# Kernel optimization log

Hardware: AMD Instinct MI355X
Metric: run time of the kernel (lower is better)

The kernel has to match this reference:

```python
import math
import jax, jax.numpy as jnp
import numpy as np

B, S, D = 2, 2048, 4096
H = 32
HD = D // H  # 128
CLIP_QKV = 8.0
ALIBI_BIAS_MAX = 8
LN_EPS = 1e-5


def _get_alibi_slopes(total_num_heads: int, alibi_bias_max: int) -> np.ndarray:
    next_pow2 = 2 ** math.ceil(math.log2(total_num_heads))
    m = np.arange(1, next_pow2 + 1, dtype=np.float32) * (alibi_bias_max / next_pow2)
    slopes = 1.0 / np.power(2.0, m)
    if next_pow2 != total_num_heads:
        slopes = np.concatenate([slopes[1::2], slopes[::2]])[:total_num_heads]
    return slopes


ALIBI_SLOPES = jnp.asarray(_get_alibi_slopes(H, ALIBI_BIAS_MAX))  # [H]


def _layernorm(x, w, b):
    mu = jnp.mean(x, axis=-1, keepdims=True)
    var = jnp.mean(jnp.square(x - mu), axis=-1, keepdims=True)
    return (x - mu) * jax.lax.rsqrt(var + LN_EPS) * w + b


def setup_inputs() -> dict:
    key = jax.random.key(0)
    ks = jax.random.split(key, 3)
    scale_in = 1.0 / math.sqrt(D)
    return {
        "hidden_states": jax.random.normal(ks[0], (B, S, D), jnp.float32),
        "Wqkv": jax.random.normal(ks[1], (D, 3 * D), jnp.float32) * scale_in,
        "Wout": jax.random.normal(ks[2], (D, D), jnp.float32) * scale_in,
        "q_ln_w": jnp.ones((D,), jnp.float32),
        "q_ln_b": jnp.zeros((D,), jnp.float32),
        "k_ln_w": jnp.ones((D,), jnp.float32),
        "k_ln_b": jnp.zeros((D,), jnp.float32),
    }


def reference(hidden_states, Wqkv, Wout, q_ln_w, q_ln_b, k_ln_w, k_ln_b):
    # QKV projection + clamp
    qkv = jnp.clip(hidden_states @ Wqkv, -CLIP_QKV, CLIP_QKV)  # [B,S,3D]
    q, k, v = jnp.split(qkv, [D, 2 * D], axis=-1)
    # QK LayerNorm over full d_model (as in MPT qk_ln)
    q = _layernorm(q, q_ln_w, q_ln_b)
    k = _layernorm(k, k_ln_w, k_ln_b)
    # split heads
    q = q.reshape(B, S, H, HD)
    k = k.reshape(B, S, H, HD)
    v = v.reshape(B, S, H, HD)
    scale = HD ** (-0.5)
    scores = jnp.einsum("bqhd,bkhd->bhqk", q, k) * scale  # [B,H,S,S]
    # ALiBi bias: -slope * (i - j), causal mask j <= i
    pos = jnp.arange(S)
    dist = pos[:, None] - pos[None, :]  # [S,S], i - j
    bias = -ALIBI_SLOPES[:, None, None] * dist.astype(jnp.float32)  # [H,S,S]
    causal = dist >= 0
    scores = jnp.where(causal[None, None], scores + bias[None], -jnp.inf)
    attn = jax.nn.softmax(scores, axis=-1)
    out = jnp.einsum("bhqk,bkhd->bqhd", attn, v).reshape(B, S, D)
    return out @ Wout
```

## Files before the change

### kernel.cpp

```cpp
#include <hip/hip_runtime.h>
#include <hip/hip_bf16.h>
#include <stdint.h>

#define BB 2
#define SS 2048
#define DD 4096
#define HH 32
#define HDD 128

typedef unsigned short u16;
typedef unsigned int u32;

constexpr float CLIPV  = 8.0f;
constexpr float LN_EPS_ = 1e-5f;
constexpr float SCALE_ = 0.08838834764831845f;
constexpr float LOG2E_ = 1.4426950408889634f;

using f32x4 = __attribute__((ext_vector_type(4))) float;
using s16x8 = __attribute__((ext_vector_type(8))) short;

__device__ inline u16 f2bf(float f) {
  union { float f; u32 u; } v; v.f = f;
  u32 r = (v.u + 0x7FFFu + ((v.u >> 16) & 1u)) >> 16;
  return (u16)r;
}
__device__ inline float bf2f(u16 u) {
  union { u32 u; float f; } v; v.u = ((u32)u) << 16;
  return v.f;
}

typedef __attribute__((address_space(1))) void gvoid;
typedef __attribute__((address_space(3))) void lvoid;
__device__ inline void gload_lds16(const void* g, void* l) {
  __builtin_amdgcn_global_load_lds((gvoid*)g, (lvoid*)l, 16, 0, 0);
}

__device__ inline f32x4 mfma16(s16x8 a, s16x8 b, f32x4 c) {
  return __builtin_amdgcn_mfma_f32_16x16x32_bf16(a, b, c, 0, 0, 0);
}

__global__ void k_cvt_bf16(const float* __restrict__ in, u16* __restrict__ out, int nvec) {
  int i = blockIdx.x * 256 + threadIdx.x;
  if (i >= nvec) return;
  float4 a = ((const float4*)in)[i * 2];
  float4 b = ((const float4*)in)[i * 2 + 1];
  u16 tmp[8];
  tmp[0] = f2bf(a.x); tmp[1] = f2bf(a.y); tmp[2] = f2bf(a.z); tmp[3] = f2bf(a.w);
  tmp[4] = f2bf(b.x); tmp[5] = f2bf(b.y); tmp[6] = f2bf(b.z); tmp[7] = f2bf(b.w);
  ((uint4*)out)[i] = *(const uint4*)tmp;
}

__global__ void k_transpose_cvt(const float* __restrict__ src, u16* __restrict__ dst, int R, int C) {
  __shared__ float tile[32][33];
  int c0 = blockIdx.x * 32, r0 = blockIdx.y * 32;
  int tx = threadIdx.x & 31, ty = threadIdx.x >> 5;
  #pragma unroll
  for (int i = 0; i < 32; i += 8)
    tile[ty + i][tx] = src[(size_t)(r0 + ty + i) * C + (c0 + tx)];
  __syncthreads();
  #pragma unroll
  for (int i = 0; i < 32; i += 8)
    dst[(size_t)(c0 + ty + i) * R + (r0 + tx)] = f2bf(tile[tx][ty + i]);
}

__device__ __forceinline__ void stage_half(u16* ldsHalf, const u16* g, int K, int tid) {
  #pragma unroll
  for (int it = 0; it < 2; ++it) {
    int p = (it << 9) + tid;
    int row = p >> 3;
    int slotk = (p & 7) ^ (row & 7);
    gload_lds16(g + (size_t)row * K + (slotk << 3), ldsHalf + ((size_t)p << 3));
  }
}

#define MFMA_QUAD(MB, JB)                                                     \
  _Pragma("unroll")                                                           \
  for (int i_ = 0; i_ < 4; ++i_) {                                            \
    _Pragma("unroll")                                                         \
    for (int jj_ = 0; jj_ < 2; ++jj_) {                                       \
      acc[(MB) + i_][(JB) + jj_] =                                            \
          mfma16(aF[i_][0], bF[(JB) + jj_][0], acc[(MB) + i_][(JB) + jj_]);   \
      acc[(MB) + i_][(JB) + jj_] =                                            \
          mfma16(aF[i_][1], bF[(JB) + jj_][1], acc[(MB) + i_][(JB) + jj_]);   \
    }                                                                         \
  }

template <int EPI>
__launch_bounds__(512)
__global__ void k_gemm256(const u16* __restrict__ A, const u16* __restrict__ Bt,
                          void* __restrict__ Cout, int M, int N, int K, int nBY) {
  __shared__ u16 sA[32768];
  __shared__ u16 sB[32768];
  const int tid = threadIdx.x;
  const int lane = tid & 63, w = tid >> 6;
  const int wm = w >> 2, wn = w & 3;
  const int lg = lane >> 4, lc = lane & 15;

  const int nwg = gridDim.x;
  const int cpx = nwg >> 3;
  const int id2 = (blockIdx.x & 7) * cpx + (blockIdx.x >> 3);
  const int bx = id2 / nBY, by = id2 % nBY;
  const int m0 = by * 256, n0 = bx * 256;

  const int NT = K >> 6;
  const u16* gA = A  + (size_t)m0 * K;
  const u16* gB = Bt + (size_t)n0 * K;

  const int xt0 = ((lg) ^ (lc & 7)) * 8;
  const int xt1 = xt0 ^ 32;
  const int rowoff = lc * 64;

  f32x4 acc[8][4];
  #pragma unroll
  for (int i = 0; i < 8; ++i)
    #pragma unroll
    for (int j = 0; j < 4; ++j) acc[i][j] = (f32x4){0.f, 0.f, 0.f, 0.f};

  stage_half(sA,        gA,                    K, tid);
  stage_half(sA + 8192, gA + (size_t)128 * K,  K, tid);
  stage_half(sB,        gB,                    K, tid);
  stage_half(sB + 8192, gB + (size_t)128 * K,  K, tid);
  if (NT > 1) {
    stage_half(sB + 16384,        gB + 64,                   K, tid);
    stage_half(sB + 16384 + 8192, gB + (size_t)128 * K + 64, K, tid);
    stage_half(sA + 16384,        gA + 64,                   K, tid);
    asm volatile("s_waitcnt vmcnt(6)" ::: "memory");
  } else {
    asm volatile("s_waitcnt vmcnt(0)" ::: "memory");
  }
  __builtin_amdgcn_s_barrier();

  for (int t = 0; t < NT; ++t) {
    const int d = t & 1;
    u16* aB = sA + d * 16384 + wm * 8192;
    u16* bB = sB + d * 16384 + (wn >> 1) * 8192 + (wn & 1) * 4096;

    s16x8 aF[4][2], bF[4][2];

    #pragma unroll
    for (int j = 0; j < 2; ++j) {
      bF[j][0] = *(const s16x8*)(bB + j * 1024 + rowoff + xt0);
      bF[j][1] = *(const s16x8*)(bB + j * 1024 + rowoff + xt1);
    }
    #pragma unroll
    for (int i = 0; i < 4; ++i) {
      aF[i][0] = *(const s16x8*)(aB + i * 1024 + rowoff + xt0);
      aF[i][1] = *(const s16x8*)(aB + i * 1024 + rowoff + xt1);
    }
    if (t + 1 < NT)
      stage_half(sA + (d ^ 1) * 16384 + 8192,
                 gA + (size_t)128 * K + (size_t)(t + 1) * 64, K, tid);
    __builtin_amdgcn_s_barrier();
    asm volatile("s_waitcnt lgkmcnt(0)" ::: "memory");
    __builtin_amdgcn_s_setprio(1);
    MFMA_QUAD(0, 0)
    __builtin_amdgcn_s_setprio(0);
    __builtin_amdgcn_s_barrier();

    #pragma unroll
    for (int j = 2; j < 4; ++j) {
      bF[j][0] = *(const s16x8*)(bB + j * 1024 + rowoff + xt0);
      bF[j][1] = *(const s16x8*)(bB + j * 1024 + rowoff + xt1);
    }
    __builtin_amdgcn_s_barrier();
    asm volatile("s_waitcnt lgkmcnt(0)" ::: "memory");
    __builtin_amdgcn_s_setprio(1);
    MFMA_QUAD(0, 2)
    __builtin_amdgcn_s_setprio(0);
    __builtin_amdgcn_s_barrier();

    #pragma unroll
    for (int i = 0; i < 4; ++i) {
      aF[i][0] = *(const s16x8*)(aB + 4096 + i * 1024 + rowoff + xt0);
      aF[i][1] = *(const s16x8*)(aB + 4096 + i * 1024 + rowoff + xt1);
    }
    if (t + 2 < NT) {
      stage_half(sB + d * 16384,        gB + (size_t)(t + 2) * 64,                   K, tid);
      stage_half(sB + d * 16384 + 8192, gB + (size_t)128 * K + (size_t)(t + 2) * 64, K, tid);
    }
    __builtin_amdgcn_s_barrier();
    asm volatile("s_waitcnt lgkmcnt(0)" ::: "memory");
    __builtin_amdgcn_s_setprio(1);
    MFMA_QUAD(4, 0)
    __builtin_amdgcn_s_setprio(0);
    __builtin_amdgcn_s_barrier();

    if (t + 2 < NT)
      stage_half(sA + d * 16384, gA + (size_t)(t + 2) * 64, K, tid);
    __builtin_amdgcn_s_barrier();
    asm volatile("s_waitcnt lgkmcnt(0)" ::: "memory");
    __builtin_amdgcn_s_setprio(1);
    MFMA_QUAD(4, 2)
    __builtin_amdgcn_s_setprio(0);
    if (t + 2 < NT) asm volatile("s_waitcnt vmcnt(6)" ::: "memory");
    else            asm volatile("s_waitcnt vmcnt(0)" ::: "memory");
    __builtin_amdgcn_s_barrier();
  }

  #pragma unroll
  for (int i = 0; i < 8; ++i)
    #pragma unroll
    for (int j = 0; j < 4; ++j)
      #pragma unroll
      for (int r = 0; r < 4; ++r) {
        int m = m0 + wm * 128 + i * 16 + lg * 4 + r;
        int n = n0 + wn * 64 + j * 16 + lc;
        float v = acc[i][j][r];
        if (EPI == 0) {
          v = fminf(fmaxf(v, -CLIPV), CLIPV);
          ((u16*)Cout)[(size_t)m * N + n] = f2bf(v);
        } else {
          ((float*)Cout)[(size_t)m * N + n] = v;
        }
      }
}

__device__ inline void unpack8(uint4 u, float* f) {
  const u16* p = (const u16*)&u;
  #pragma unroll
  for (int j = 0; j < 8; ++j) f[j] = bf2f(p[j]);
}

__global__ void k_ln_reorder(const u16* __restrict__ qkv,
                             const float* __restrict__ qw, const float* __restrict__ qb,
                             const float* __restrict__ kw, const float* __restrict__ kb,
                             u16* __restrict__ Qo, u16* __restrict__ Ko) {
  const int row = blockIdx.x;
  const int b = row >> 11, s = row & 2047;
  const int t = threadIdx.x;
  const int lane = t & 63, w = t >> 6;
  const uint4* base = (const uint4*)(qkv + (size_t)row * (3 * DD));

  __shared__ float redsum[8], redss[8];

  uint4 q4[2], k4[2];
  q4[0] = base[t];        q4[1] = base[256 + t];
  k4[0] = base[512 + t];  k4[1] = base[768 + t];

  float qx[16], kx[16];
  unpack8(q4[0], qx); unpack8(q4[1], qx + 8);
  unpack8(k4[0], kx); unpack8(k4[1], kx + 8);

  float qs = 0.f, qss = 0.f, ks = 0.f, kss = 0.f;
  #pragma unroll
  for (int i = 0; i < 16; ++i) {
    qs += qx[i]; qss += qx[i] * qx[i];
    ks += kx[i]; kss += kx[i] * kx[i];
  }
  #pragma unroll
  for (int off = 1; off < 64; off <<= 1) {
    qs  += __shfl_xor(qs, off);  qss += __shfl_xor(qss, off);
    ks  += __shfl_xor(ks, off);  kss += __shfl_xor(kss, off);
  }
  if (lane == 0) { redsum[w] = qs; redss[w] = qss; redsum[4 + w] = ks; redss[4 + w] = kss; }
  __syncthreads();
  float qsum = redsum[0] + redsum[1] + redsum[2] + redsum[3];
  float qs2  = redss[0]  + redss[1]  + redss[2]  + redss[3];
  float ksum = redsum[4] + redsum[5] + redsum[6] + redsum[7];
  float ks2  = redss[4]  + redss[5]  + redss[6]  + redss[7];
  const float inv = 1.0f / (float)DD;
  float qmu = qsum * inv, qvar = qs2 * inv - qmu * qmu;
  float kmu = ksum * inv, kvar = ks2 * inv - kmu * kmu;
  float qrs = rsqrtf(qvar + LN_EPS_);
  float krs = rsqrtf(kvar + LN_EPS_);

  #pragma unroll
  for (int ch = 0; ch < 2; ++ch) {
    int c0 = ch * 2048 + t * 8;
    int hh = c0 >> 7, hd0 = c0 & 127;
    size_t idx = (((size_t)b * HH + hh) * SS + s) * HDD + hd0;
    {
      float4 w0 = *(const float4*)(qw + c0), w1 = *(const float4*)(qw + c0 + 4);
      float4 b0 = *(const float4*)(qb + c0), b1 = *(const float4*)(qb + c0 + 4);
      float wa[8] = {w0.x, w0.y, w0.z, w0.w, w1.x, w1.y, w1.z, w1.w};
      float ba[8] = {b0.x, b0.y, b0.z, b0.w, b1.x, b1.y, b1.z, b1.w};
      u16 tmp[8];
      #pragma unroll
      for (int j = 0; j < 8; ++j)
        tmp[j] = f2bf((qx[ch * 8 + j] - qmu) * qrs * wa[j] + ba[j]);
      *(uint4*)(Qo + idx) = *(const uint4*)tmp;
    }
    {
      float4 w0 = *(const float4*)(kw + c0), w1 = *(const float4*)(kw + c0 + 4);
      float4 b0 = *(const float4*)(kb + c0), b1 = *(const float4*)(kb + c0 + 4);
      float wa[8] = {w0.x, w0.y, w0.z, w0.w, w1.x, w1.y, w1.z, w1.w};
      float ba[8] = {b0.x, b0.y, b0.z, b0.w, b1.x, b1.y, b1.z, b1.w};
      u16 tmp[8];
      #pragma unroll
      for (int j = 0; j < 8; ++j)
        tmp[j] = f2bf((kx[ch * 8 + j] - kmu) * krs * wa[j] + ba[j]);
      *(uint4*)(Ko + idx) = *(const uint4*)tmp;
    }
  }
}

__global__ void k_transpose_v(const u16* __restrict__ qkv, u16* __restrict__ Vt) {
  __shared__ u16 ls[64 * 65];
  const int s0 = blockIdx.x * 64;
  const int hd0 = blockIdx.y * 64;
  const int bh = blockIdx.z;
  const int b = bh >> 5, h = bh & 31;
  const int t = threadIdx.x;
  const u16* src = qkv + (size_t)(b * SS + s0) * (3 * DD) + 2 * DD + h * HDD + hd0;
  #pragma unroll
  for (int it = 0; it < 4; ++it) {
    int idx = it * 256 + t;
    int sr = idx >> 4, hc = idx & 15;
    uint2 v = *(const uint2*)(src + (size_t)sr * (3 * DD) + hc * 4);
    const u16* pv = (const u16*)&v;
    #pragma unroll
    for (int j = 0; j < 4; ++j) ls[sr * 65 + hc * 4 + j] = pv[j];
  }
  __syncthreads();
  u16* dst = Vt + ((size_t)bh * HDD + hd0) * SS + s0;
  #pragma unroll
  for (int it = 0; it < 4; ++it) {
    int idx = it * 256 + t;
    int hd = idx >> 4, sc = idx & 15;
    u16 tmp[4];
    #pragma unroll
    for (int j = 0; j < 4; ++j) tmp[j] = ls[(4 * sc + j) * 65 + hd];
    *(uint2*)(dst + (size_t)hd * SS + 4 * sc) = *(const uint2*)tmp;
  }
}

__global__ void k_attn(const u16* __restrict__ Qg, const u16* __restrict__ Kg,
                       const u16* __restrict__ Vt, u16* __restrict__ Og) {
  const int qt = blockIdx.x;
  const int bh = blockIdx.y;
  const int b = bh >> 5, h = bh & 31;
  const int t = threadIdx.x;
  const int lane = t & 63, w = t >> 6;
  const int lg = lane >> 4, lc = lane & 15;
  const float slope = exp2f(-0.25f * (float)(h + 1));

  __shared__ u16 lK[8192];
  __shared__ u16 lV[8192];
  __shared__ u16 lP[4][1024];

  const int q0 = qt * 64 + w * 16;
  const size_t bhS = (size_t)bh * SS;
  const u16* Kbase = Kg + bhS * HDD;
  const u16* Vbase = Vt + bhS * HDD;

  s16x8 qf[4];
  {
    const u16* qrow = Qg + (bhS + q0 + lc) * HDD;
    #pragma unroll
    for (int kt = 0; kt < 4; ++kt) qf[kt] = *(const s16x8*)(qrow + kt * 32 + lg * 8);
  }

  f32x4 ot[8];
  #pragma unroll
  for (int hf = 0; hf < 8; ++hf) ot[hf] = (f32x4){0.f, 0.f, 0.f, 0.f};
  float m_r = -1e30f, l_r = 0.f;

  for (int kv0 = 0; kv0 <= qt * 64; kv0 += 64) {
    #pragma unroll
    for (int it = 0; it < 4; ++it) {
      int sl = it * 256 + t;
      int row = sl >> 4, k16 = sl & 15;
      gload_lds16(Kbase + (size_t)(kv0 + row) * HDD + ((k16 ^ (row & 7)) * 8),
                  &lK[sl * 8]);
    }
    #pragma unroll
    for (int it = 0; it < 4; ++it) {
      int sl = it * 256 + t;
      int row = sl >> 3, k8 = sl & 7;
      gload_lds16(Vbase + (size_t)row * SS + kv0 + ((k8 ^ (row & 7)) * 8),
                  &lV[sl * 8]);
    }
    __syncthreads();

    f32x4 st[4];
    #pragma unroll
    for (int i = 0; i < 4; ++i) {
      st[i] = (f32x4){0.f, 0.f, 0.f, 0.f};
      #pragma unroll
      for (int kt = 0; kt < 4; ++kt) {
        int r = i * 16 + lc;
        const s16x8 ka = *(const s16x8*)&lK[r * 128 + (((kt * 4 + lg) ^ (r & 7)) * 8)];
        st[i] = mfma16(ka, qf[kt], st[i]);
      }
    }

    float sc[4][4];
    float pm = -1e30f;
    const int qg = q0 + lc;
    #pragma unroll
    for (int i = 0; i < 4; ++i)
      #pragma unroll
      for (int r = 0; r < 4; ++r) {
        int kv = kv0 + i * 16 + lg * 4 + r;
        float x = (kv <= qg) ? st[i][r] * SCALE_ - slope * (float)(qg - kv) : -1e30f;
        sc[i][r] = x;
        pm = fmaxf(pm, x);
      }
    pm = fmaxf(pm, __shfl_xor(pm, 16));
    pm = fmaxf(pm, __shfl_xor(pm, 32));
    float m_new = fmaxf(m_r, pm);
    float alpha = exp2f((m_r - m_new) * LOG2E_);
    float rsum = 0.f;
    #pragma unroll
    for (int i = 0; i < 4; ++i) {
      float p0 = exp2f((sc[i][0] - m_new) * LOG2E_);
      float p1 = exp2f((sc[i][1] - m_new) * LOG2E_);
      float p2 = exp2f((sc[i][2] - m_new) * LOG2E_);
      float p3 = exp2f((sc[i][3] - m_new) * LOG2E_);
      rsum += (p0 + p1) + (p2 + p3);
      u32 dlo, dhi;
      asm("v_cvt_pk_bf16_f32 %0, %1, %2" : "=v"(dlo) : "v"(p0), "v"(p1));
      asm("v_cvt_pk_bf16_f32 %0, %1, %2" : "=v"(dhi) : "v"(p2), "v"(p3));
      int addr = lc * 64 + (((4 * i + lg) ^ (2 * (lc & 7))) * 4);
      uint2 val; val.x = dlo; val.y = dhi;
      *(uint2*)&lP[w][addr] = val;
    }
    rsum += __shfl_xor(rsum, 16);
    rsum += __shfl_xor(rsum, 32);
    l_r = l_r * alpha + rsum;
    m_r = m_new;

    #pragma unroll
    for (int hf = 0; hf < 8; ++hf) {
      ot[hf][0] *= alpha; ot[hf][1] *= alpha; ot[hf][2] *= alpha; ot[hf][3] *= alpha;
    }

    #pragma unroll
    for (int ks = 0; ks < 2; ++ks) {
      const int m = 4 * ks + lg;
      const s16x8 pa = *(const s16x8*)&lP[w][lc * 64 + ((m ^ (lc & 7)) * 8)];
      #pragma unroll
      for (int hf = 0; hf < 8; ++hf) {
        int row = hf * 16 + lc;
        const s16x8 vb = *(const s16x8*)&lV[row * 64 + ((m ^ (row & 7)) * 8)];
        ot[hf] = mfma16(vb, pa, ot[hf]);
      }
    }
    __syncthreads();
  }

  float linv = 1.f / l_r;
  const size_t obase = ((size_t)(b * SS + q0 + lc)) * DD + h * HDD;
  #pragma unroll
  for (int hf = 0; hf < 8; ++hf) {
    u16 tmp[4];
    #pragma unroll
    for (int r = 0; r < 4; ++r) tmp[r] = f2bf(ot[hf][r] * linv);
    *(uint2*)&Og[obase + hf * 16 + lg * 4] = *(const uint2*)tmp;
  }
}

extern "C" void kernel_launch(void* const* d_in, const int* in_sizes, int n_in,
                              void* d_out, int out_size, void* d_ws, size_t ws_size,
                              hipStream_t stream) {
  const float* hidden = (const float*)d_in[0];
  const float* Wqkv   = (const float*)d_in[1];
  const float* Wout   = (const float*)d_in[2];
  const float* qw     = (const float*)d_in[3];
  const float* qb     = (const float*)d_in[4];
  const float* kw     = (const float*)d_in[5];
  const float* kb     = (const float*)d_in[6];
  float* out = (float*)d_out;
  char* ws = (char*)d_ws;

  u16* Xb    = (u16*)(ws);
  u16* WqkvT = (u16*)(ws + 33554432);
  u16* Qb    = (u16*)(ws + 33554432);
  u16* Kb    = (u16*)(ws + 67108864);
  u16* Vtb   = (u16*)(ws + 100663296);
  u16* WoutT = (u16*)(ws + 134217728);
  u16* qkv   = (u16*)(ws + 167772160);
  u16* attnO = Xb;

  k_cvt_bf16<<<8192, 256, 0, stream>>>(hidden, Xb, 2097152);
  k_transpose_cvt<<<dim3(12288 / 32, 4096 / 32), 256, 0, stream>>>(Wqkv, WqkvT, 4096, 12288);
  k_transpose_cvt<<<dim3(4096 / 32, 4096 / 32), 256, 0, stream>>>(Wout, WoutT, 4096, 4096);
  k_gemm256<0><<<768, 512, 0, stream>>>(Xb, WqkvT, qkv, 4096, 12288, 4096, 16);
  k_ln_reorder<<<4096, 256, 0, stream>>>(qkv, qw, qb, kw, kb, Qb, Kb);
  k_transpose_v<<<dim3(SS / 64, HDD / 64, BB * HH), 256, 0, stream>>>(qkv, Vtb);
  k_attn<<<dim3(32, 64), 256, 0, stream>>>(Qb, Kb, Vtb, attnO);
  k_gemm256<1><<<256, 512, 0, stream>>>(attnO, WoutT, out, 4096, 4096, 4096, 16);
}
```

Before: 893.7 us.

## Double-buffer K/V tiles in attention, remap blocks, and restructure GEMM A-tile prefetch

The attention kernel now double-buffers K and V tiles in shared memory, issuing async loads for the next KV tile before computing the current one, so global-load latency overlaps with MFMA work. The launch grid becomes 1D with a block-ID remap that interleaves heads and query tiles across XCD-like groups, aiming at better load balance and cache locality. In the GEMM, the second half of the A tile is now prefetched two iterations ahead together with the first half instead of one iteration ahead, with the vmcnt waits adjusted to match. Shared memory per attention block doubles, which may reduce occupancy.

Measured after the change: 882.8 us. No clear change (-1.2%).

```diff
diff --git a/kernel.cpp b/kernel.cpp
--- a/kernel.cpp
+++ b/kernel.cpp
@@ -124,7 +124,8 @@
     stage_half(sB + 16384,        gB + 64,                   K, tid);
     stage_half(sB + 16384 + 8192, gB + (size_t)128 * K + 64, K, tid);
     stage_half(sA + 16384,        gA + 64,                   K, tid);
-    asm volatile("s_waitcnt vmcnt(6)" ::: "memory");
+    stage_half(sA + 16384 + 8192, gA + (size_t)128 * K + 64, K, tid);
+    asm volatile("s_waitcnt vmcnt(8)" ::: "memory");
   } else {
     asm volatile("s_waitcnt vmcnt(0)" ::: "memory");
   }
@@ -147,9 +148,6 @@
       aF[i][0] = *(const s16x8*)(aB + i * 1024 + rowoff + xt0);
       aF[i][1] = *(const s16x8*)(aB + i * 1024 + rowoff + xt1);
     }
-    if (t + 1 < NT)
-      stage_half(sA + (d ^ 1) * 16384 + 8192,
-                 gA + (size_t)128 * K + (size_t)(t + 1) * 64, K, tid);
     __builtin_amdgcn_s_barrier();
     asm volatile("s_waitcnt lgkmcnt(0)" ::: "memory");
     __builtin_amdgcn_s_setprio(1);
@@ -185,14 +183,16 @@
     __builtin_amdgcn_s_setprio(0);
     __builtin_amdgcn_s_barrier();
 
-    if (t + 2 < NT)
-      stage_half(sA + d * 16384, gA + (size_t)(t + 2) * 64, K, tid);
+    if (t + 2 < NT) {
+      stage_half(sA + d * 16384,        gA + (size_t)(t + 2) * 64,                   K, tid);
+      stage_half(sA + d * 16384 + 8192, gA + (size_t)128 * K + (size_t)(t + 2) * 64, K, tid);
+    }
     __builtin_amdgcn_s_barrier();
     asm volatile("s_waitcnt lgkmcnt(0)" ::: "memory");
     __builtin_amdgcn_s_setprio(1);
     MFMA_QUAD(4, 2)
     __builtin_amdgcn_s_setprio(0);
-    if (t + 2 < NT) asm volatile("s_waitcnt vmcnt(6)" ::: "memory");
+    if (t + 2 < NT) asm volatile("s_waitcnt vmcnt(8)" ::: "memory");
     else            asm volatile("s_waitcnt vmcnt(0)" ::: "memory");
     __builtin_amdgcn_s_barrier();
   }
@@ -324,18 +324,21 @@
   }
 }
 
-__global__ void k_attn(const u16* __restrict__ Qg, const u16* __restrict__ Kg,
-                       const u16* __restrict__ Vt, u16* __restrict__ Og) {
-  const int qt = blockIdx.x;
-  const int bh = blockIdx.y;
+__global__ __launch_bounds__(256)
+void k_attn(const u16* __restrict__ Qg, const u16* __restrict__ Kg,
+            const u16* __restrict__ Vt, u16* __restrict__ Og) {
+  const int bid = blockIdx.x;
+  const int id2 = ((bid & 7) << 8) + (bid >> 3);
+  const int bh = id2 >> 5;
+  const int qt = id2 & 31;
   const int b = bh >> 5, h = bh & 31;
   const int t = threadIdx.x;
   const int lane = t & 63, w = t >> 6;
   const int lg = lane >> 4, lc = lane & 15;
   const float slope = exp2f(-0.25f * (float)(h + 1));
 
-  __shared__ u16 lK[8192];
-  __shared__ u16 lV[8192];
+  __shared__ u16 lK[2][8192];
+  __shared__ u16 lV[2][8192];
   __shared__ u16 lP[4][1024];
 
   const int q0 = qt * 64 + w * 16;
@@ -355,22 +358,32 @@
   for (int hf = 0; hf < 8; ++hf) ot[hf] = (f32x4){0.f, 0.f, 0.f, 0.f};
   float m_r = -1e30f, l_r = 0.f;
 
-  for (int kv0 = 0; kv0 <= qt * 64; kv0 += 64) {
-    #pragma unroll
-    for (int it = 0; it < 4; ++it) {
-      int sl = it * 256 + t;
-      int row = sl >> 4, k16 = sl & 15;
-      gload_lds16(Kbase + (size_t)(kv0 + row) * HDD + ((k16 ^ (row & 7)) * 8),
-                  &lK[sl * 8]);
-    }
-    #pragma unroll
-    for (int it = 0; it < 4; ++it) {
-      int sl = it * 256 + t;
-      int row = sl >> 3, k8 = sl & 7;
-      gload_lds16(Vbase + (size_t)row * SS + kv0 + ((k8 ^ (row & 7)) * 8),
-                  &lV[sl * 8]);
-    }
-    __syncthreads();
+  #define STAGE_KV(D, KV0)                                                         \
+    {                                                                              \
+      _Pragma("unroll")                                                            \
+      for (int it_ = 0; it_ < 4; ++it_) {                                          \
+        int sl = it_ * 256 + t;                                                    \
+        int row = sl >> 4, k16 = sl & 15;                                          \
+        gload_lds16(Kbase + (size_t)((KV0) + row) * HDD + ((k16 ^ (row & 7)) * 8), \
+                    &lK[D][sl * 8]);                                               \
+      }                                                                            \
+      _Pragma("unroll")                                                            \
+      for (int it_ = 0; it_ < 4; ++it_) {                                          \
+        int sl = it_ * 256 + t;                                                    \
+        int row = sl >> 3, k8 = sl & 7;                                            \
+        gload_lds16(Vbase + (size_t)row * SS + (KV0) + ((k8 ^ (row & 7)) * 8),     \
+                    &lV[D][sl * 8]);                                               \
+      }                                                                            \
+    }
+
+  STAGE_KV(0, 0)
+  __syncthreads();
+
+  const int nt = qt + 1;
+  for (int itn = 0; itn < nt; ++itn) {
+    const int d = itn & 1;
+    const int kv0 = itn * 64;
+    if (itn + 1 < nt) STAGE_KV(d ^ 1, kv0 + 64)
 
     f32x4 st[4];
     #pragma unroll
@@ -379,7 +392,7 @@
       #pragma unroll
       for (int kt = 0; kt < 4; ++kt) {
         int r = i * 16 + lc;
-        const s16x8 ka = *(const s16x8*)&lK[r * 128 + (((kt * 4 + lg) ^ (r & 7)) * 8)];
+        const s16x8 ka = *(const s16x8*)&lK[d][r * 128 + (((kt * 4 + lg) ^ (r & 7)) * 8)];
         st[i] = mfma16(ka, qf[kt], st[i]);
       }
     }
@@ -432,12 +445,13 @@
       #pragma unroll
       for (int hf = 0; hf < 8; ++hf) {
         int row = hf * 16 + lc;
-        const s16x8 vb = *(const s16x8*)&lV[row * 64 + ((m ^ (row & 7)) * 8)];
+        const s16x8 vb = *(const s16x8*)&lV[d][row * 64 + ((m ^ (row & 7)) * 8)];
         ot[hf] = mfma16(vb, pa, ot[hf]);
       }
     }
     __syncthreads();
   }
+  #undef STAGE_KV
 
   float linv = 1.f / l_r;
   const size_t obase = ((size_t)(b * SS + q0 + lc)) * DD + h * HDD;
@@ -478,6 +492,6 @@
   k_gemm256<0><<<768, 512, 0, stream>>>(Xb, WqkvT, qkv, 4096, 12288, 4096, 16);
   k_ln_reorder<<<4096, 256, 0, stream>>>(qkv, qw, qb, kw, kb, Qb, Kb);
   k_transpose_v<<<dim3(SS / 64, HDD / 64, BB * HH), 256, 0, stream>>>(qkv, Vtb);
-  k_attn<<<dim3(32, 64), 256, 0, stream>>>(Qb, Kb, Vtb, attnO);
+  k_attn<<<2048, 256, 0, stream>>>(Qb, Kb, Vtb, attnO);
   k_gemm256<1><<<256, 512, 0, stream>>>(attnO, WoutT, out, 4096, 4096, 4096, 16);
 }
```
